# Optimization experiments

Measured on AMD Instinct MI355X. Metric: run time of the kernel, lower is better.

## Reference

```python
import jax, jax.numpy as jnp
import numpy as np

N_NODES = 50000
N_EDGES = 800000
NODE_DIM = 64
EDGE_DIM = 32
OUT_FEATS = 64


def setup_inputs() -> dict:
    key = jax.random.key(0)
    k1, k2, k3, k4, k5, k6, k7 = jax.random.split(key, 7)
    node_features = jax.random.normal(k1, (N_NODES, NODE_DIM), dtype=jnp.float32)
    edge_features = jax.random.normal(k2, (N_EDGES, EDGE_DIM), dtype=jnp.float32)
    src = jax.random.randint(k3, (N_EDGES,), 0, N_NODES, dtype=jnp.int32)
    dst = jax.random.randint(k4, (N_EDGES,), 0, N_NODES, dtype=jnp.int32)
    in_dim = 2 * NODE_DIM + EDGE_DIM  # concat([e_ft, h_src, h_dst])
    w_group = jax.random.normal(k5, (in_dim,), dtype=jnp.float32) * 0.05
    w_srcattn = jax.random.normal(k6, (NODE_DIM + EDGE_DIM,), dtype=jnp.float32) * 0.05
    w_lin = jax.random.normal(k7, (in_dim, OUT_FEATS), dtype=jnp.float32) * 0.05
    return {"node_features": node_features, "edge_features": edge_features,
            "src": src, "dst": dst,
            "w_group": w_group, "w_srcattn": w_srcattn, "w_lin": w_lin}


def _segment_softmax(scores, seg, num_segments):
    # numerically-stable softmax of per-edge scalar scores within each segment
    m = jax.ops.segment_max(scores, seg, num_segments=num_segments)
    e = jnp.exp(scores - m[seg])
    s = jax.ops.segment_sum(e, seg, num_segments=num_segments)
    return e / s[seg]


def reference(node_features, edge_features, src, dst, w_group, w_srcattn, w_lin):
    h = node_features              # [N, node_dim]
    e_ft = edge_features           # [E, edge_dim]
    h_src = h[src]                 # [E, node_dim]
    h_dst = h[dst]                 # [E, node_dim]

    # --- group_apply_edges(group_by='src'): edge attention over out-edges of each src ---
    z2 = jnp.concatenate([e_ft, h_src, h_dst], axis=1)      # [E, edge_dim + 2*node_dim]
    a = z2 @ w_group                                        # [E]
    gamma = _segment_softmax(a, src, N_NODES)               # softmax over edges sharing src
    e_weighted = gamma[:, None] * e_ft                      # [E, edge_dim]

    # --- gnn_msg: msg = concat([h_src, e_weighted]) ---
    msg = jnp.concatenate([h_src, e_weighted], axis=1)      # [E, node_dim + edge_dim]

    # --- gnn_reduce: attention softmax over mailbox (edges sharing dst), weighted sum ---
    s = msg @ w_srcattn                                     # [E]
    alpha = _segment_softmax(s, dst, N_NODES)
    accum = jax.ops.segment_sum(alpha[:, None] * msg, dst, num_segments=N_NODES)  # [N, node_dim+edge_dim]

    # --- node_update: linear(concat([h, accum])) + relu ---
    h_cat = jnp.concatenate([h, accum], axis=1)             # [N, 2*node_dim + edge_dim]
    out = jax.nn.relu(h_cat @ w_lin)                        # [N, out_feats]
    return out
```

## Files before the change

### kernel.cpp

```cpp
#include <hip/hip_runtime.h>

#define NN 50000
#define NE 800000
#define NEB 3125
#define NHB 3125
#define NTILES 3125

typedef __attribute__((ext_vector_type(8))) short bf16x8;
typedef __attribute__((ext_vector_type(4))) short s16x4;
typedef __attribute__((ext_vector_type(4))) float f32x4;

static __device__ __forceinline__ short f2bf(float f) {
    unsigned int u = __float_as_uint(f);
    u += 0x7FFFu + ((u >> 16) & 1u);
    return (short)(u >> 16);
}

__global__ __launch_bounds__(256) void k_hist(
    const int* __restrict__ dst, int* __restrict__ cnt, int* __restrict__ rank)
{
    int e = blockIdx.x * 256 + threadIdx.x;
    if (e < NE) rank[e] = atomicAdd(&cnt[dst[e]], 1);
}

__global__ __launch_bounds__(256) void k_proj(
    const float* __restrict__ h, const float* __restrict__ wg,
    const float* __restrict__ wa, float* __restrict__ p1,
    int2* __restrict__ pdo, float* __restrict__ dpf, short* __restrict__ hb)
{
    __shared__ float4 ls[16], ld[16], lt[16];
    int tid = threadIdx.x;
    if (tid < 16)      ls[tid]      = ((const float4*)wg)[8 + tid];
    else if (tid < 32) ld[tid - 16] = ((const float4*)wg)[8 + tid];
    else if (tid < 48) lt[tid - 32] = ((const float4*)wa)[tid - 32];
    __syncthreads();
    int n = blockIdx.x * 16 + (tid >> 4);
    if (n >= NN) return;
    int l16 = tid & 15;
    float4 v = ((const float4*)(h + (size_t)n * 64))[l16];
    s16x4 hv;
    hv[0] = f2bf(v.x); hv[1] = f2bf(v.y); hv[2] = f2bf(v.z); hv[3] = f2bf(v.w);
    *(s16x4*)(hb + (size_t)n * 160 + l16 * 4) = hv;
    float4 w1 = ls[l16], w2 = ld[l16], w3 = lt[l16];
    float s1 = v.x*w1.x + v.y*w1.y + v.z*w1.z + v.w*w1.w;
    float s2 = v.x*w2.x + v.y*w2.y + v.z*w2.z + v.w*w2.w;
    float s3 = v.x*w3.x + v.y*w3.y + v.z*w3.z + v.w*w3.w;
    #pragma unroll
    for (int m = 8; m; m >>= 1) {
        s1 += __shfl_xor(s1, m);
        s2 += __shfl_xor(s2, m);
        s3 += __shfl_xor(s3, m);
    }
    if (l16 == 0) {
        p1[n] = s1;
        pdo[n].x = __float_as_int(s2);
        dpf[2 * n + 1] = s3;
    }
}

__global__ __launch_bounds__(256) void k_assign(
    const int* __restrict__ cnt, int2* __restrict__ pdo, int* __restrict__ gtotal)
{
    int n = blockIdx.x * 256 + threadIdx.x;
    int lane = threadIdx.x & 63;
    int c = (n < NN) ? cnt[n] : 0;
    int pre = c;
    #pragma unroll
    for (int d = 1; d < 64; d <<= 1) {
        int v = __shfl_up(pre, d);
        if (lane >= d) pre += v;
    }
    int base = 0;
    if (lane == 63) base = atomicAdd(gtotal, pre);
    base = __shfl(base, 63);
    if (n < NN) pdo[n].y = base + pre - c;
}

__global__ __launch_bounds__(256) void k_edge(
    const float* __restrict__ ef, const int* __restrict__ src,
    const int* __restrict__ dst, const int* __restrict__ rank,
    const float* __restrict__ wg, const float* __restrict__ wa,
    const float* __restrict__ p1, const int2* __restrict__ pdo,
    float* __restrict__ dpf, int* __restrict__ eidx,
    float2* __restrict__ recB)
{
    __shared__ float4 lwe[8], lae[8];
    int tid = threadIdx.x;
    if (tid < 8)       lwe[tid]     = ((const float4*)wg)[tid];
    else if (tid < 16) lae[tid - 8] = ((const float4*)wa)[tid - 8 + 16];
    __syncthreads();
    int e = blockIdx.x * 256 + tid;
    if (e >= NE) return;
    int s = src[e], d = dst[e], rk = rank[e];
    float p1v = p1[s];
    int2 pv = pdo[d];
    float pdv = __int_as_float(pv.x);
    int pos = pv.y + rk;
    const float4* e4 = (const float4*)(ef + (size_t)e * 32);
    float a = 0.f, u = 0.f;
    #pragma unroll
    for (int q = 0; q < 8; ++q) {
        float4 v = e4[q], w = lwe[q], w2 = lae[q];
        a += v.x*w.x  + v.y*w.y  + v.z*w.z  + v.w*w.w;
        u += v.x*w2.x + v.y*w2.y + v.z*w2.z + v.w*w2.w;
    }
    float ev = __expf(a + p1v + pdv);
    atomicAdd(&dpf[2 * s], ev);
    recB[e] = make_float2(ev, u);
    eidx[pos] = e;
}

__global__ __launch_bounds__(256) void k_reduce(
    const float* __restrict__ h, const float* __restrict__ ef,
    const int* __restrict__ src, const int* __restrict__ cnt,
    const int2* __restrict__ pdo, const float2* __restrict__ dp,
    const int* __restrict__ eidx, const float2* __restrict__ recB,
    short* __restrict__ hb)
{
    int n = blockIdx.x * 4 + (threadIdx.x >> 6);
    if (n >= NN) return;
    int lane = threadIdx.x & 63;
    bool up = lane >= 32;
    int l5 = lane & 31;
    int deg = cnt[n], base = pdo[n].y;
    const int* ep = eidx + base;
    float acch = 0.f, acce = 0.f, den = 0.f;
    int j = 0;
    for (; j + 8 <= deg; j += 8) {
        int e[8];
        #pragma unroll
        for (int t = 0; t < 8; ++t) e[t] = ep[j + t];
        float2 rb[8]; int sv[8];
        #pragma unroll
        for (int t = 0; t < 8; ++t) { rb[t] = recB[e[t]]; sv[t] = src[e[t]]; }
        float2 dv[8]; float hv[8];
        #pragma unroll
        for (int t = 0; t < 8; ++t) {
            dv[t] = dp[sv[t]];
            hv[t] = h[((unsigned)sv[t] << 6) + lane];
        }
        float efv[4];
        #pragma unroll
        for (int t = 0; t < 4; ++t) {
            int ee = up ? e[2*t+1] : e[2*t];
            efv[t] = ef[((unsigned)ee << 5) + l5];
        }
        float g[8], s[8];
        #pragma unroll
        for (int t = 0; t < 8; ++t) {
            g[t] = rb[t].x * __builtin_amdgcn_rcpf(dv[t].x);
            s[t] = __expf(dv[t].y + g[t] * rb[t].y);
            den  += s[t];
            acch += s[t] * hv[t];
        }
        #pragma unroll
        for (int t = 0; t < 4; ++t) {
            float w = up ? s[2*t+1]*g[2*t+1] : s[2*t]*g[2*t];
            acce += w * efv[t];
        }
    }
    if (j + 4 <= deg) {
        int e[4];
        #pragma unroll
        for (int t = 0; t < 4; ++t) e[t] = ep[j + t];
        float2 rb[4]; int sv[4];
        #pragma unroll
        for (int t = 0; t < 4; ++t) { rb[t] = recB[e[t]]; sv[t] = src[e[t]]; }
        float2 dv[4]; float hv[4];
        #pragma unroll
        for (int t = 0; t < 4; ++t) {
            dv[t] = dp[sv[t]];
            hv[t] = h[((unsigned)sv[t] << 6) + lane];
        }
        float efv[2];
        #pragma unroll
        for (int t = 0; t < 2; ++t) {
            int ee = up ? e[2*t+1] : e[2*t];
            efv[t] = ef[((unsigned)ee << 5) + l5];
        }
        float g[4], s[4];
        #pragma unroll
        for (int t = 0; t < 4; ++t) {
            g[t] = rb[t].x * __builtin_amdgcn_rcpf(dv[t].x);
            s[t] = __expf(dv[t].y + g[t] * rb[t].y);
            den  += s[t];
            acch += s[t] * hv[t];
        }
        #pragma unroll
        for (int t = 0; t < 2; ++t) {
            float w = up ? s[2*t+1]*g[2*t+1] : s[2*t]*g[2*t];
            acce += w * efv[t];
        }
        j += 4;
    }
    for (; j < deg; ++j) {
        int e = ep[j];
        float2 rb = recB[e];
        int s0 = src[e];
        float2 dt = dp[s0];
        float g = rb.x * __builtin_amdgcn_rcpf(dt.x);
        float sx = __expf(dt.y + g * rb.y);
        den += sx;
        acch += sx * h[((unsigned)s0 << 6) + lane];
        if (!up) acce += sx * g * ef[((unsigned)e << 5) + l5];
    }
    acce += __shfl_xor(acce, 32);
    float inv = (deg > 0) ? __builtin_amdgcn_rcpf(den) : 0.f;
    size_t hbase = (size_t)n * 160;
    hb[hbase + 64 + lane] = f2bf(acch * inv);
    if (!up) hb[hbase + 128 + l5] = f2bf(acce * inv);
}

__global__ __launch_bounds__(256) void k_node_update(
    const short* __restrict__ hb, const float* __restrict__ wl_g,
    float* __restrict__ out)
{
    int lane = threadIdx.x & 63;
    int col  = lane & 15;
    int quad = lane >> 4;
    int tile = blockIdx.x * 4 + (threadIdx.x >> 6);
    if (tile >= NTILES) return;

    bf16x8 bfr[5][4];
    #pragma unroll
    for (int kc = 0; kc < 5; ++kc)
        #pragma unroll
        for (int nt = 0; nt < 4; ++nt) {
            #pragma unroll
            for (int j = 0; j < 8; ++j) {
                int k = kc * 32 + quad * 8 + j;
                bfr[kc][nt][j] = f2bf(wl_g[k * 64 + nt * 16 + col]);
            }
        }

    int n = tile * 16 + col;
    f32x4 acc[4];
    #pragma unroll
    for (int nt = 0; nt < 4; ++nt) acc[nt] = (f32x4){0.f, 0.f, 0.f, 0.f};

    const short* hrow = hb + (size_t)n * 160 + quad * 8;
    #pragma unroll
    for (int kc = 0; kc < 5; ++kc) {
        bf16x8 af = *(const bf16x8*)(hrow + kc * 32);
        #pragma unroll
        for (int nt = 0; nt < 4; ++nt)
            acc[nt] = __builtin_amdgcn_mfma_f32_16x16x32_bf16(
                af, bfr[kc][nt], acc[nt], 0, 0, 0);
    }

    #pragma unroll
    for (int nt = 0; nt < 4; ++nt) {
        #pragma unroll
        for (int r = 0; r < 4; ++r) {
            int node = tile * 16 + quad * 4 + r;
            out[(size_t)node * 64 + nt * 16 + col] = fmaxf(acc[nt][r], 0.f);
        }
    }
}

extern "C" void kernel_launch(void* const* d_in, const int* in_sizes, int n_in,
                              void* d_out, int out_size, void* d_ws, size_t ws_size,
                              hipStream_t stream)
{
    const float* h   = (const float*)d_in[0];
    const float* ef  = (const float*)d_in[1];
    const int*   src = (const int*)d_in[2];
    const int*   dst = (const int*)d_in[3];
    const float* wg  = (const float*)d_in[4];
    const float* wa  = (const float*)d_in[5];
    const float* wl  = (const float*)d_in[6];
    float* out = (float*)d_out;

    float*  ws     = (float*)d_ws;
    float*  dpf    = ws;
    int*    cnt    = (int*)(ws + 2 * NN);
    int*    gtotal = (int*)(ws + 3 * NN);
    int2*   pdo    = (int2*)(ws + 3 * NN + 16);
    float*  p1     = ws + 5 * NN + 16;
    int*    rank   = (int*)(ws + 6 * NN + 16);
    int*    eidx   = (int*)(ws + 6 * NN + 16 + NE);
    float2* recB   = (float2*)(ws + 6 * NN + 16 + 2 * NE);
    short*  hb     = (short*)(ws + 6 * NN + 16 + 4 * NE);

    hipMemsetAsync(d_ws, 0, (size_t)(3 * NN + 16) * sizeof(float), stream);

    k_hist<<<NEB, 256, 0, stream>>>(dst, cnt, rank);
    k_proj<<<NHB, 256, 0, stream>>>(h, wg, wa, p1, pdo, dpf, hb);
    k_assign<<<(NN + 255) / 256, 256, 0, stream>>>(cnt, pdo, gtotal);
    k_edge<<<NEB, 256, 0, stream>>>(ef, src, dst, rank, wg, wa, p1, pdo,
                                    dpf, eidx, recB);
    k_reduce<<<(NN + 3) / 4, 256, 0, stream>>>(h, ef, src, cnt, pdo,
                                               (const float2*)dpf, eidx, recB, hb);
    k_node_update<<<782, 256, 0, stream>>>(hb, wl, out);
}
```

Before: 352.7 us.

## Pack per-edge records by destination and fuse histogram with node projection

Merges the degree histogram and node projection into one launch, and drops the per-edge rank array in favour of an atomic cursor per destination. Edge records (src, edge id, exp score, edge attention term) are now written as one 16-byte struct in destination-sorted order, so the reduce reads them contiguously instead of chasing eidx then recB and src. The reduce also gathers neighbour features from the bf16 copy in hb instead of fp32 h, which halves gather bytes at some precision cost. The cursor atomics make record order within a segment nondeterministic.

```diff
diff --git a/kernel.cpp b/kernel.cpp
--- a/kernel.cpp
+++ b/kernel.cpp
@@ -9,32 +9,35 @@
 typedef __attribute__((ext_vector_type(8))) short bf16x8;
 typedef __attribute__((ext_vector_type(4))) short s16x4;
 typedef __attribute__((ext_vector_type(4))) float f32x4;
+typedef __attribute__((ext_vector_type(4))) int   i32x4;
 
 static __device__ __forceinline__ short f2bf(float f) {
     unsigned int u = __float_as_uint(f);
     u += 0x7FFFu + ((u >> 16) & 1u);
     return (short)(u >> 16);
 }
-
-__global__ __launch_bounds__(256) void k_hist(
-    const int* __restrict__ dst, int* __restrict__ cnt, int* __restrict__ rank)
-{
-    int e = blockIdx.x * 256 + threadIdx.x;
-    if (e < NE) rank[e] = atomicAdd(&cnt[dst[e]], 1);
-}
-
-__global__ __launch_bounds__(256) void k_proj(
-    const float* __restrict__ h, const float* __restrict__ wg,
-    const float* __restrict__ wa, float* __restrict__ p1,
-    int2* __restrict__ pdo, float* __restrict__ dpf, short* __restrict__ hb)
-{
+static __device__ __forceinline__ float bf2f(short b) {
+    return __uint_as_float(((unsigned)(unsigned short)b) << 16);
+}
+
+__global__ __launch_bounds__(256) void k_pre(
+    const float* __restrict__ h, const int* __restrict__ dst,
+    const float* __restrict__ wg, const float* __restrict__ wa,
+    int* __restrict__ cnt, float* __restrict__ p1, float* __restrict__ pd,
+    float* __restrict__ dpf, short* __restrict__ hb)
+{
+    int tid = threadIdx.x;
+    if (blockIdx.x < NEB) {
+        int e = blockIdx.x * 256 + tid;
+        if (e < NE) atomicAdd(&cnt[dst[e]], 1);
+        return;
+    }
     __shared__ float4 ls[16], ld[16], lt[16];
-    int tid = threadIdx.x;
     if (tid < 16)      ls[tid]      = ((const float4*)wg)[8 + tid];
     else if (tid < 32) ld[tid - 16] = ((const float4*)wg)[8 + tid];
     else if (tid < 48) lt[tid - 32] = ((const float4*)wa)[tid - 32];
     __syncthreads();
-    int n = blockIdx.x * 16 + (tid >> 4);
+    int n = (blockIdx.x - NEB) * 16 + (tid >> 4);
     if (n >= NN) return;
     int l16 = tid & 15;
     float4 v = ((const float4*)(h + (size_t)n * 64))[l16];
@@ -51,15 +54,12 @@
         s2 += __shfl_xor(s2, m);
         s3 += __shfl_xor(s3, m);
     }
-    if (l16 == 0) {
-        p1[n] = s1;
-        pdo[n].x = __float_as_int(s2);
-        dpf[2 * n + 1] = s3;
-    }
+    if (l16 == 0) { p1[n] = s1; pd[n] = s2; dpf[2 * n + 1] = s3; }
 }
 
 __global__ __launch_bounds__(256) void k_assign(
-    const int* __restrict__ cnt, int2* __restrict__ pdo, int* __restrict__ gtotal)
+    const int* __restrict__ cnt, int* __restrict__ off, int* __restrict__ cursor,
+    int* __restrict__ gtotal)
 {
     int n = blockIdx.x * 256 + threadIdx.x;
     int lane = threadIdx.x & 63;
@@ -73,16 +73,15 @@
     int base = 0;
     if (lane == 63) base = atomicAdd(gtotal, pre);
     base = __shfl(base, 63);
-    if (n < NN) pdo[n].y = base + pre - c;
+    if (n < NN) { int b = base + pre - c; off[n] = b; cursor[n] = b; }
 }
 
 __global__ __launch_bounds__(256) void k_edge(
     const float* __restrict__ ef, const int* __restrict__ src,
-    const int* __restrict__ dst, const int* __restrict__ rank,
-    const float* __restrict__ wg, const float* __restrict__ wa,
-    const float* __restrict__ p1, const int2* __restrict__ pdo,
-    float* __restrict__ dpf, int* __restrict__ eidx,
-    float2* __restrict__ recB)
+    const int* __restrict__ dst, const float* __restrict__ wg,
+    const float* __restrict__ wa, const float* __restrict__ p1,
+    const float* __restrict__ pd, float* __restrict__ dpf,
+    int* __restrict__ cursor, i32x4* __restrict__ recA)
 {
     __shared__ float4 lwe[8], lae[8];
     int tid = threadIdx.x;
@@ -91,11 +90,8 @@
     __syncthreads();
     int e = blockIdx.x * 256 + tid;
     if (e >= NE) return;
-    int s = src[e], d = dst[e], rk = rank[e];
-    float p1v = p1[s];
-    int2 pv = pdo[d];
-    float pdv = __int_as_float(pv.x);
-    int pos = pv.y + rk;
+    int s = src[e], d = dst[e];
+    float p1v = p1[s], pdv = pd[d];
     const float4* e4 = (const float4*)(ef + (size_t)e * 32);
     float a = 0.f, u = 0.f;
     #pragma unroll
@@ -106,50 +102,46 @@
     }
     float ev = __expf(a + p1v + pdv);
     atomicAdd(&dpf[2 * s], ev);
-    recB[e] = make_float2(ev, u);
-    eidx[pos] = e;
+    int pos = atomicAdd(&cursor[d], 1);
+    recA[pos] = (i32x4){s, e, __float_as_int(ev), __float_as_int(u)};
 }
 
 __global__ __launch_bounds__(256) void k_reduce(
-    const float* __restrict__ h, const float* __restrict__ ef,
-    const int* __restrict__ src, const int* __restrict__ cnt,
-    const int2* __restrict__ pdo, const float2* __restrict__ dp,
-    const int* __restrict__ eidx, const float2* __restrict__ recB,
-    short* __restrict__ hb)
+    const float* __restrict__ ef, const int* __restrict__ off,
+    const int* __restrict__ cursor, const float2* __restrict__ dp,
+    const i32x4* __restrict__ recA, short* __restrict__ hb)
 {
     int n = blockIdx.x * 4 + (threadIdx.x >> 6);
     if (n >= NN) return;
     int lane = threadIdx.x & 63;
     bool up = lane >= 32;
     int l5 = lane & 31;
-    int deg = cnt[n], base = pdo[n].y;
-    const int* ep = eidx + base;
+    int base = off[n];
+    int deg = cursor[n] - base;
+    const i32x4* rp = recA + base;
     float acch = 0.f, acce = 0.f, den = 0.f;
     int j = 0;
     for (; j + 8 <= deg; j += 8) {
-        int e[8];
-        #pragma unroll
-        for (int t = 0; t < 8; ++t) e[t] = ep[j + t];
-        float2 rb[8]; int sv[8];
-        #pragma unroll
-        for (int t = 0; t < 8; ++t) { rb[t] = recB[e[t]]; sv[t] = src[e[t]]; }
+        i32x4 r[8];
+        #pragma unroll
+        for (int t = 0; t < 8; ++t) r[t] = rp[j + t];
         float2 dv[8]; float hv[8];
         #pragma unroll
         for (int t = 0; t < 8; ++t) {
-            dv[t] = dp[sv[t]];
-            hv[t] = h[((unsigned)sv[t] << 6) + lane];
+            dv[t] = dp[r[t][0]];
+            hv[t] = bf2f(hb[(size_t)(unsigned)r[t][0] * 160 + lane]);
         }
         float efv[4];
         #pragma unroll
         for (int t = 0; t < 4; ++t) {
-            int ee = up ? e[2*t+1] : e[2*t];
+            int ee = up ? r[2*t+1][1] : r[2*t][1];
             efv[t] = ef[((unsigned)ee << 5) + l5];
         }
         float g[8], s[8];
         #pragma unroll
         for (int t = 0; t < 8; ++t) {
-            g[t] = rb[t].x * __builtin_amdgcn_rcpf(dv[t].x);
-            s[t] = __expf(dv[t].y + g[t] * rb[t].y);
+            g[t] = __int_as_float(r[t][2]) * __builtin_amdgcn_rcpf(dv[t].x);
+            s[t] = __expf(dv[t].y + g[t] * __int_as_float(r[t][3]));
             den  += s[t];
             acch += s[t] * hv[t];
         }
@@ -160,29 +152,26 @@
         }
     }
     if (j + 4 <= deg) {
-        int e[4];
-        #pragma unroll
-        for (int t = 0; t < 4; ++t) e[t] = ep[j + t];
-        float2 rb[4]; int sv[4];
-        #pragma unroll
-        for (int t = 0; t < 4; ++t) { rb[t] = recB[e[t]]; sv[t] = src[e[t]]; }
+        i32x4 r[4];
+        #pragma unroll
+        for (int t = 0; t < 4; ++t) r[t] = rp[j + t];
         float2 dv[4]; float hv[4];
         #pragma unroll
         for (int t = 0; t < 4; ++t) {
-            dv[t] = dp[sv[t]];
-            hv[t] = h[((unsigned)sv[t] << 6) + lane];
+            dv[t] = dp[r[t][0]];
+            hv[t] = bf2f(hb[(size_t)(unsigned)r[t][0] * 160 + lane]);
         }
         float efv[2];
         #pragma unroll
         for (int t = 0; t < 2; ++t) {
-            int ee = up ? e[2*t+1] : e[2*t];
+            int ee = up ? r[2*t+1][1] : r[2*t][1];
             efv[t] = ef[((unsigned)ee << 5) + l5];
         }
         float g[4], s[4];
         #pragma unroll
         for (int t = 0; t < 4; ++t) {
-            g[t] = rb[t].x * __builtin_amdgcn_rcpf(dv[t].x);
-            s[t] = __expf(dv[t].y + g[t] * rb[t].y);
+            g[t] = __int_as_float(r[t][2]) * __builtin_amdgcn_rcpf(dv[t].x);
+            s[t] = __expf(dv[t].y + g[t] * __int_as_float(r[t][3]));
             den  += s[t];
             acch += s[t] * hv[t];
         }
@@ -194,15 +183,13 @@
         j += 4;
     }
     for (; j < deg; ++j) {
-        int e = ep[j];
-        float2 rb = recB[e];
-        int s0 = src[e];
-        float2 dt = dp[s0];
-        float g = rb.x * __builtin_amdgcn_rcpf(dt.x);
-        float sx = __expf(dt.y + g * rb.y);
+        i32x4 r = rp[j];
+        float2 dt = dp[r[0]];
+        float g = __int_as_float(r[2]) * __builtin_amdgcn_rcpf(dt.x);
+        float sx = __expf(dt.y + g * __int_as_float(r[3]));
         den += sx;
-        acch += sx * h[((unsigned)s0 << 6) + lane];
-        if (!up) acce += sx * g * ef[((unsigned)e << 5) + l5];
+        acch += sx * bf2f(hb[(size_t)(unsigned)r[0] * 160 + lane]);
+        if (!up) acce += sx * g * ef[((unsigned)r[1] << 5) + l5];
     }
     acce += __shfl_xor(acce, 32);
     float inv = (deg > 0) ? __builtin_amdgcn_rcpf(den) : 0.f;
@@ -275,21 +262,20 @@
     float*  dpf    = ws;
     int*    cnt    = (int*)(ws + 2 * NN);
     int*    gtotal = (int*)(ws + 3 * NN);
-    int2*   pdo    = (int2*)(ws + 3 * NN + 16);
+    int*    off    = (int*)(ws + 3 * NN + 16);
+    int*    cursor = (int*)(ws + 4 * NN + 16);
     float*  p1     = ws + 5 * NN + 16;
-    int*    rank   = (int*)(ws + 6 * NN + 16);
-    int*    eidx   = (int*)(ws + 6 * NN + 16 + NE);
-    float2* recB   = (float2*)(ws + 6 * NN + 16 + 2 * NE);
-    short*  hb     = (short*)(ws + 6 * NN + 16 + 4 * NE);
+    float*  pd     = ws + 6 * NN + 16;
+    i32x4*  recA   = (i32x4*)(ws + 7 * NN + 16);
+    short*  hb     = (short*)(ws + 7 * NN + 16 + 4 * NE);
 
     hipMemsetAsync(d_ws, 0, (size_t)(3 * NN + 16) * sizeof(float), stream);
 
-    k_hist<<<NEB, 256, 0, stream>>>(dst, cnt, rank);
-    k_proj<<<NHB, 256, 0, stream>>>(h, wg, wa, p1, pdo, dpf, hb);
-    k_assign<<<(NN + 255) / 256, 256, 0, stream>>>(cnt, pdo, gtotal);
-    k_edge<<<NEB, 256, 0, stream>>>(ef, src, dst, rank, wg, wa, p1, pdo,
-                                    dpf, eidx, recB);
-    k_reduce<<<(NN + 3) / 4, 256, 0, stream>>>(h, ef, src, cnt, pdo,
-                                               (const float2*)dpf, eidx, recB, hb);
+    k_pre<<<NEB + NHB, 256, 0, stream>>>(h, dst, wg, wa, cnt, p1, pd, dpf, hb);
+    k_assign<<<(NN + 255) / 256, 256, 0, stream>>>(cnt, off, cursor, gtotal);
+    k_edge<<<NEB, 256, 0, stream>>>(ef, src, dst, wg, wa, p1, pd, dpf,
+                                    cursor, recA);
+    k_reduce<<<(NN + 3) / 4, 256, 0, stream>>>(ef, off, cursor,
+                                               (const float2*)dpf, recA, hb);
     k_node_update<<<782, 256, 0, stream>>>(hb, wl, out);
 }
```

Result: slower. 360.8 us (+2.3%).
